# Optimization experiments

Measured on AMD Instinct MI355X. Metric: run time of the kernel, lower is better.

Reference implementation:

```python
import jax, jax.numpy as jnp
import numpy as np
import math

N = 50000        # nodes
E = 800000       # edges (avg degree 16)
NFEAT = 512
NHID = 512
NCLASS = 128


def setup_inputs() -> dict:
    key = jax.random.key(0)
    ks = jax.random.split(key, 8)
    x = jax.random.normal(ks[0], (N, NFEAT), dtype=jnp.float32)
    edge_src = jax.random.randint(ks[1], (E,), 0, N)
    edge_dst = jax.random.randint(ks[2], (E,), 0, N)
    edge_w = jax.random.uniform(ks[3], (E,), dtype=jnp.float32)
    s1 = 1.0 / math.sqrt(NFEAT)
    s2 = 1.0 / math.sqrt(NHID)
    # torch Linear weight layout: [out_features, in_features]
    W1 = jax.random.uniform(ks[4], (NHID, NFEAT), dtype=jnp.float32, minval=-s1, maxval=s1)
    b1 = jax.random.uniform(ks[5], (NHID,), dtype=jnp.float32, minval=-s1, maxval=s1)
    W2 = jax.random.uniform(ks[6], (NCLASS, NHID), dtype=jnp.float32, minval=-s2, maxval=s2)
    b2 = jax.random.uniform(ks[7], (NCLASS,), dtype=jnp.float32, minval=-s2, maxval=s2)
    return {"x": x, "edge_w": edge_w, "W1": W1, "b1": b1, "W2": W2, "b2": b2,
            "edge_src": edge_src, "edge_dst": edge_dst}


def reference(x, edge_w, W1, b1, W2, b2, edge_src, edge_dst):
    # spmm(adj, support): out[i] = sum_{e: src[e]==i} w[e] * support[dst[e]]
    def spmm(support):
        gathered = edge_w[:, None] * support[edge_dst]  # [E, F]
        return jax.ops.segment_sum(gathered, edge_src, num_segments=N)

    # layer 1: linear -> spmm -> relu (dropout is identity in eval mode)
    h = spmm(x @ W1.T + b1)
    h = jax.nn.relu(h)
    # layer 2 (output layer): linear -> spmm
    out = spmm(h @ W2.T + b2)
    return out
```

## Files before the change

kernel.cpp:

```cpp
#include <hip/hip_runtime.h>
#include <hip/hip_bf16.h>
#include <hip/hip_fp8.h>
#include <stdint.h>

#define N_NODES 50000
#define N_EDGES 800000
#define NFEAT 512
#define NHID 512
#define NCLASS 128
#define MPAD 50048

#define CONVX_BLOCKS 12512
#define CONVW1_BLOCKS 128
#define CONVW2_BLOCKS 32
#define HIST_BLOCKS 3125
#define G1_BM 391
#define G1_BLOCKS 1564
#define FILL_BLOCKS 3125

typedef short short8 __attribute__((ext_vector_type(8)));
typedef float f32x4 __attribute__((ext_vector_type(4)));
typedef float f32x2 __attribute__((ext_vector_type(2)));

__device__ __forceinline__ ushort f2bf(float f) {
  union { float f; uint32_t u; } v; v.f = f;
  uint32_t u = v.u;
  uint32_t r = (u + 0x7fffu + ((u >> 16) & 1u)) >> 16;
  return (ushort)r;
}
__device__ __forceinline__ float bf2f(ushort h) {
  union { uint32_t u; float f; } v; v.u = ((uint32_t)h) << 16;
  return v.f;
}

__device__ __forceinline__ uint8_t enc_fp8(float f) {
#if __has_builtin(__builtin_amdgcn_cvt_pk_fp8_f32)
  int r = __builtin_amdgcn_cvt_pk_fp8_f32(f, f, 0, false);
  return (uint8_t)(r & 0xff);
#else
  __hip_fp8_e4m3 t(f);
  return t.__x;
#endif
}
__device__ __forceinline__ float dec_fp8_byte(uint32_t b) {
  uint32_t e = (b >> 3) & 15u, m = b & 7u, s = (b & 0x80u) << 24;
  union { uint32_t u; float f; } n; n.u = s | ((e + 120u) << 23) | (m << 20);
  union { uint32_t u; float f; } d; d.f = (float)m * 0x1p-9f; d.u |= s;
  return e ? n.f : d.f;
}

__device__ __forceinline__ void acc_fp8x4(float* a, uint32_t v, float w) {
#if __has_builtin(__builtin_amdgcn_cvt_pk_f32_fp8)
  f32x2 lo = __builtin_amdgcn_cvt_pk_f32_fp8(v, false);
  f32x2 hi = __builtin_amdgcn_cvt_pk_f32_fp8(v, true);
  a[0] += w * lo[0]; a[1] += w * lo[1]; a[2] += w * hi[0]; a[3] += w * hi[1];
#else
  a[0] += w * dec_fp8_byte(v & 0xffu);
  a[1] += w * dec_fp8_byte((v >> 8) & 0xffu);
  a[2] += w * dec_fp8_byte((v >> 16) & 0xffu);
  a[3] += w * dec_fp8_byte(v >> 24);
#endif
}

__device__ __forceinline__ void acc_bf16x2(float* a, uint32_t v, float w) {
  a[0] += w * bf2f((ushort)(v & 0xffffu));
  a[1] += w * bf2f((ushort)(v >> 16));
}

__device__ __forceinline__ void conv8(const float* __restrict__ in,
                                      ushort* __restrict__ out, long idx) {
  const float4* p = (const float4*)(in + idx);
  float4 a = p[0], b = p[1];
  short8 o;
  o[0] = f2bf(a.x); o[1] = f2bf(a.y); o[2] = f2bf(a.z); o[3] = f2bf(a.w);
  o[4] = f2bf(b.x); o[5] = f2bf(b.y); o[6] = f2bf(b.z); o[7] = f2bf(b.w);
  *(short8*)(out + idx) = o;
}

__device__ __forceinline__ void gload_lds16(const void* g, void* lds) {
  __builtin_amdgcn_global_load_lds(
      (const __attribute__((address_space(1))) void*)g,
      (__attribute__((address_space(3))) void*)lds,
      16, 0, 0);
}

__global__ __launch_bounds__(256) void k_prep(const float* __restrict__ x,
                                              ushort* __restrict__ xb,
                                              const float* __restrict__ W1,
                                              ushort* __restrict__ w1b,
                                              const float* __restrict__ W2,
                                              ushort* __restrict__ w2b) {
  int b = blockIdx.x, t = threadIdx.x;
  if (b < CONVX_BLOCKS) {
    long idx = ((long)b * 256 + t) * 8;
    int row = (int)(idx >> 9);
    if (row < N_NODES) {
      conv8(x, xb, idx);
    } else {
      *(short8*)(xb + idx) = (short8)0;
    }
  } else if (b < CONVX_BLOCKS + CONVW1_BLOCKS) {
    long idx = ((long)(b - CONVX_BLOCKS) * 256 + t) * 8;
    conv8(W1, w1b, idx);
  } else {
    long idx = ((long)(b - CONVX_BLOCKS - CONVW1_BLOCKS) * 256 + t) * 8;
    conv8(W2, w2b, idx);
  }
}

__global__ __launch_bounds__(256) void k_alloc(const int* __restrict__ deg,
                                               int* __restrict__ rpb,
                                               int* __restrict__ rpe,
                                               int* __restrict__ counter) {
  int i = blockIdx.x * blockDim.x + threadIdx.x;
  int lane = threadIdx.x & 63;
  int d = (i < N_NODES) ? deg[i] : 0;
  int sc = d;
  #pragma unroll
  for (int off = 1; off < 64; off <<= 1) {
    int u = __shfl_up(sc, off, 64);
    if (lane >= off) sc += u;
  }
  int base = 0;
  if (lane == 63) base = atomicAdd(counter, sc);
  base = __shfl(base, 63, 64);
  if (i < N_NODES) {
    int start = base + sc - d;
    rpb[i] = start;
    rpe[i] = start + d;
  }
}

__global__ __launch_bounds__(256) void k_fill(const int* __restrict__ src,
                                              const int* __restrict__ dst,
                                              const float* __restrict__ w,
                                              const int* __restrict__ rpb,
                                              const int* __restrict__ rank,
                                              uint2* __restrict__ esw) {
  int e = blockIdx.x * blockDim.x + threadIdx.x;
  if (e < N_EDGES) {
    int pos = rpb[src[e]] + rank[e];
    uint2 p;
    p.x = (unsigned)dst[e];
    p.y = __float_as_uint(w[e]);
    esw[pos] = p;
  }
}

template <int OUT_FP8>
__device__ __forceinline__ void gemm_body(const ushort* __restrict__ A,
                                          const ushort* __restrict__ B,
                                          const float* __restrict__ bias,
                                          void* __restrict__ Cout,
                                          int K, int Nout, int bm, int bn,
                                          ushort* sA, ushort* sB) {
  const int t = threadIdx.x;
  const int lane = t & 63;
  const int wave = t >> 6;
  const int wr = wave >> 1, wc = wave & 1;

  f32x4 acc[4][4];
  #pragma unroll
  for (int i = 0; i < 4; i++)
    #pragma unroll
    for (int j = 0; j < 4; j++) acc[i][j] = (f32x4)0.f;

  const long a_base = (long)bm * 128 * K;
  const long b_base = (long)bn * 128 * K;

  for (int kt = 0; kt < K; kt += 64) {
    #pragma unroll
    for (int it = 0; it < 4; ++it) {
      int c = it * 256 + t;
      int r = c >> 3, ccp = c & 7;
      int cc = ccp ^ (r & 7);
      const ushort* ga = A + a_base + (long)r * K + kt + cc * 8;
      const ushort* gb = B + b_base + (long)r * K + kt + cc * 8;
      char* la = (char*)sA + (it * 256 + wave * 64) * 16;
      char* lb = (char*)sB + (it * 256 + wave * 64) * 16;
      gload_lds16(ga, la);
      gload_lds16(gb, lb);
    }
    __syncthreads();
    #pragma unroll
    for (int kk = 0; kk < 2; ++kk) {
      short8 af[4], bfr[4];
      int kchunk = kk * 4 + (lane >> 4);
      #pragma unroll
      for (int mr = 0; mr < 4; ++mr) {
        int row = wr * 64 + mr * 16 + (lane & 15);
        af[mr] = *(const short8*)((const char*)sA + row * 128 +
                                  ((kchunk * 16) ^ ((row & 7) << 4)));
      }
      #pragma unroll
      for (int nr = 0; nr < 4; ++nr) {
        int row = wc * 64 + nr * 16 + (lane & 15);
        bfr[nr] = *(const short8*)((const char*)sB + row * 128 +
                                   ((kchunk * 16) ^ ((row & 7) << 4)));
      }
      #pragma unroll
      for (int mr = 0; mr < 4; ++mr)
        #pragma unroll
        for (int nr = 0; nr < 4; ++nr)
          acc[mr][nr] = __builtin_amdgcn_mfma_f32_16x16x32_bf16(af[mr], bfr[nr],
                                                                acc[mr][nr], 0, 0, 0);
    }
    __syncthreads();
  }

  #pragma unroll
  for (int mr = 0; mr < 4; ++mr)
    #pragma unroll
    for (int nr = 0; nr < 4; ++nr) {
      int col = bn * 128 + wc * 64 + nr * 16 + (lane & 15);
      float bv = bias[col];
      #pragma unroll
      for (int reg = 0; reg < 4; ++reg) {
        int row = bm * 128 + wr * 64 + mr * 16 + (lane >> 4) * 4 + reg;
        float val = acc[mr][nr][reg] + bv;
        if (OUT_FP8) {
          ((uint8_t*)Cout)[(long)row * Nout + col] = enc_fp8(val);
        } else {
          ((ushort*)Cout)[(long)row * Nout + col] = f2bf(val);
        }
      }
    }
}

__global__ __launch_bounds__(256) void k_gemm1_hist(const ushort* __restrict__ A,
                                                    const ushort* __restrict__ B,
                                                    const float* __restrict__ bias,
                                                    uint8_t* __restrict__ C,
                                                    const int* __restrict__ src,
                                                    int* __restrict__ deg,
                                                    int* __restrict__ rank) {
  __shared__ ushort sA[128 * 64];
  __shared__ ushort sB[128 * 64];
  int b = blockIdx.x;
  if (b < G1_BLOCKS) {
    gemm_body<1>(A, B, bias, C, NFEAT, NHID, b % G1_BM, b / G1_BM, sA, sB);
  } else {
    int e = (b - G1_BLOCKS) * 256 + threadIdx.x;
    if (e < N_EDGES) rank[e] = atomicAdd(&deg[src[e]], 1);
  }
}

__global__ __launch_bounds__(256) void k_gemm2(const ushort* __restrict__ A,
                                               const ushort* __restrict__ B,
                                               const float* __restrict__ bias,
                                               ushort* __restrict__ C) {
  __shared__ ushort sA[128 * 64];
  __shared__ ushort sB[128 * 64];
  gemm_body<0>(A, B, bias, C, NHID, NCLASS, blockIdx.x, 0, sA, sB);
}

__global__ __launch_bounds__(256) void k_spmm1(const int* __restrict__ rpb,
                                               const int* __restrict__ rpe,
                                               const uint2* __restrict__ esw,
                                               const uint8_t* __restrict__ c1,
                                               ushort* __restrict__ h) {
  int node = blockIdx.x * 4 + (threadIdx.x >> 6);
  int lane = threadIdx.x & 63;
  int half = lane >> 5;
  int col = (lane & 31) * 16;
  float a[16];
  #pragma unroll
  for (int k = 0; k < 16; ++k) a[k] = 0.f;
  if (node < N_NODES) {
    int beg = rpb[node], end = rpe[node];
    for (int j = beg; j < end; j += 8) {
      #pragma unroll
      for (int s = 0; s < 4; ++s) {
        int ei = j + s * 2 + half;
        bool vld = ei < end;
        uint2 p = esw[vld ? ei : 0];
        int d = (int)p.x;
        float w = vld ? __uint_as_float(p.y) : 0.f;
        uint4 q = *(const uint4*)(c1 + (long)d * NHID + col);
        acc_fp8x4(a, q.x, w);      acc_fp8x4(a + 4, q.y, w);
        acc_fp8x4(a + 8, q.z, w);  acc_fp8x4(a + 12, q.w, w);
      }
    }
  }
  #pragma unroll
  for (int k = 0; k < 16; ++k) a[k] += __shfl_xor(a[k], 32, 64);
  if (half == 0) {
    short8 o0, o1;
    #pragma unroll
    for (int k = 0; k < 8; ++k) {
      o0[k] = (short)f2bf(a[k] > 0.f ? a[k] : 0.f);
      o1[k] = (short)f2bf(a[k + 8] > 0.f ? a[k + 8] : 0.f);
    }
    *(short8*)(h + (long)node * NHID + col) = o0;
    *(short8*)(h + (long)node * NHID + col + 8) = o1;
  }
}

__global__ __launch_bounds__(256) void k_spmm2(const int* __restrict__ rpb,
                                               const int* __restrict__ rpe,
                                               const uint2* __restrict__ esw,
                                               const ushort* __restrict__ c2,
                                               float* __restrict__ out) {
  int node = blockIdx.x * 4 + (threadIdx.x >> 6);
  int lane = threadIdx.x & 63;
  int half = lane >> 5;
  int col = (lane & 31) * 4;
  if (node >= N_NODES) return;
  float a[4] = {0.f, 0.f, 0.f, 0.f};
  int beg = rpb[node], end = rpe[node];
  for (int j = beg; j < end; j += 8) {
    #pragma unroll
    for (int s = 0; s < 4; ++s) {
      int ei = j + s * 2 + half;
      bool vld = ei < end;
      uint2 p = esw[vld ? ei : 0];
      int d = (int)p.x;
      float w = vld ? __uint_as_float(p.y) : 0.f;
      uint2 q = *(const uint2*)(c2 + (long)d * NCLASS + col);
      acc_bf16x2(a, q.x, w);
      acc_bf16x2(a + 2, q.y, w);
    }
  }
  #pragma unroll
  for (int k = 0; k < 4; ++k) a[k] += __shfl_xor(a[k], 32, 64);
  if (half == 0) {
    f32x4 st; st[0] = a[0]; st[1] = a[1]; st[2] = a[2]; st[3] = a[3];
    *(f32x4*)(out + (long)node * NCLASS + col) = st;
  }
}

extern "C" void kernel_launch(void* const* d_in, const int* in_sizes, int n_in,
                              void* d_out, int out_size, void* d_ws, size_t ws_size,
                              hipStream_t stream) {
  const float* x    = (const float*)d_in[0];
  const float* ew   = (const float*)d_in[1];
  const float* W1   = (const float*)d_in[2];
  const float* b1   = (const float*)d_in[3];
  const float* W2   = (const float*)d_in[4];
  const float* b2   = (const float*)d_in[5];
  const int*   esrc = (const int*)d_in[6];
  const int*   edst = (const int*)d_in[7];
  float* out = (float*)d_out;

  char* ws = (char*)d_ws;
  size_t off = 0;
  auto alloc = [&](size_t bytes) -> void* {
    void* p = ws + off;
    off = (off + bytes + 255) & ~(size_t)255;
    return p;
  };

  ushort*  buf0 = (ushort*)alloc((size_t)MPAD * 512 * 2);
  uint8_t* c1f8 = (uint8_t*)alloc((size_t)MPAD * 512);
  ushort*  c2bf = (ushort*)alloc((size_t)MPAD * 128 * 2);
  ushort*  w1b  = (ushort*)alloc((size_t)512 * 512 * 2);
  ushort*  w2b  = (ushort*)alloc((size_t)128 * 512 * 2);
  int*     deg  = (int*)alloc((size_t)N_NODES * 4);
  int*     rpb  = (int*)alloc((size_t)N_NODES * 4);
  int*     rpe  = (int*)alloc((size_t)N_NODES * 4);
  int*     rank = (int*)alloc((size_t)N_EDGES * 4);
  int*     cnt  = (int*)alloc(256);
  uint2*   esw  = (uint2*)alloc((size_t)N_EDGES * 8);

  hipMemsetAsync(deg, 0, (size_t)N_NODES * 4, stream);
  hipMemsetAsync(cnt, 0, 4, stream);

  k_prep<<<CONVX_BLOCKS + CONVW1_BLOCKS + CONVW2_BLOCKS, 256, 0, stream>>>(
      x, buf0, W1, w1b, W2, w2b);

  k_gemm1_hist<<<G1_BLOCKS + HIST_BLOCKS, 256, 0, stream>>>(
      buf0, w1b, b1, c1f8, esrc, deg, rank);

  k_alloc<<<(N_NODES + 255) / 256, 256, 0, stream>>>(deg, rpb, rpe, cnt);

  k_fill<<<FILL_BLOCKS, 256, 0, stream>>>(esrc, edst, ew, rpb, rank, esw);

  k_spmm1<<<MPAD / 4, 256, 0, stream>>>(rpb, rpe, esw, c1f8, buf0);

  k_gemm2<<<G1_BM, 256, 0, stream>>>(buf0, w2b, b2, c2bf);

  k_spmm2<<<(N_NODES + 3) / 4, 256, 0, stream>>>(rpb, rpe, esw, c2bf, out);
}
```

Baseline: 249.4 us.

## Fuse x fp32-to-bf16 conversion into GEMM1 tile loads and interleave histogram blocks

Removes the separate pass that converted x to bf16 and instead converts fp32 rows on the fly while staging the A tile into LDS in GEMM1. Histogram blocks are interleaved with GEMM blocks (one GEMM to two hist) to mix compute and atomic work. This avoids writing and rereading a bf16 copy of x, at the cost of reading fp32 x once per column tile and losing async global-to-LDS loads for A.

```diff
diff --git a/kernel.cpp b/kernel.cpp
--- a/kernel.cpp
+++ b/kernel.cpp
@@ -10,12 +10,12 @@
 #define NCLASS 128
 #define MPAD 50048
 
-#define CONVX_BLOCKS 12512
 #define CONVW1_BLOCKS 128
 #define CONVW2_BLOCKS 32
 #define HIST_BLOCKS 3125
 #define G1_BM 391
 #define G1_BLOCKS 1564
+#define G1H_BLOCKS 4692
 #define FILL_BLOCKS 3125
 
 typedef short short8 __attribute__((ext_vector_type(8)));
@@ -84,26 +84,16 @@
       16, 0, 0);
 }
 
-__global__ __launch_bounds__(256) void k_prep(const float* __restrict__ x,
-                                              ushort* __restrict__ xb,
-                                              const float* __restrict__ W1,
-                                              ushort* __restrict__ w1b,
-                                              const float* __restrict__ W2,
-                                              ushort* __restrict__ w2b) {
+__global__ __launch_bounds__(256) void k_prepw(const float* __restrict__ W1,
+                                               ushort* __restrict__ w1b,
+                                               const float* __restrict__ W2,
+                                               ushort* __restrict__ w2b) {
   int b = blockIdx.x, t = threadIdx.x;
-  if (b < CONVX_BLOCKS) {
+  if (b < CONVW1_BLOCKS) {
     long idx = ((long)b * 256 + t) * 8;
-    int row = (int)(idx >> 9);
-    if (row < N_NODES) {
-      conv8(x, xb, idx);
-    } else {
-      *(short8*)(xb + idx) = (short8)0;
-    }
-  } else if (b < CONVX_BLOCKS + CONVW1_BLOCKS) {
-    long idx = ((long)(b - CONVX_BLOCKS) * 256 + t) * 8;
     conv8(W1, w1b, idx);
   } else {
-    long idx = ((long)(b - CONVX_BLOCKS - CONVW1_BLOCKS) * 256 + t) * 8;
+    long idx = ((long)(b - CONVW1_BLOCKS) * 256 + t) * 8;
     conv8(W2, w2b, idx);
   }
 }
@@ -147,13 +137,13 @@
   }
 }
 
-template <int OUT_FP8>
-__device__ __forceinline__ void gemm_body(const ushort* __restrict__ A,
-                                          const ushort* __restrict__ B,
-                                          const float* __restrict__ bias,
-                                          void* __restrict__ Cout,
-                                          int K, int Nout, int bm, int bn,
-                                          ushort* sA, ushort* sB) {
+__device__ __forceinline__ void gemm1_body(const float* __restrict__ X,
+                                           const ushort* __restrict__ B,
+                                           const float* __restrict__ bias,
+                                           uint8_t* __restrict__ Cout,
+                                           int bm, int bn,
+                                           ushort* sA, ushort* sB) {
+  const int K = NFEAT, Nout = NHID;
   const int t = threadIdx.x;
   const int lane = t & 63;
   const int wave = t >> 6;
@@ -165,21 +155,27 @@
     #pragma unroll
     for (int j = 0; j < 4; j++) acc[i][j] = (f32x4)0.f;
 
-  const long a_base = (long)bm * 128 * K;
   const long b_base = (long)bn * 128 * K;
 
   for (int kt = 0; kt < K; kt += 64) {
     #pragma unroll
     for (int it = 0; it < 4; ++it) {
       int c = it * 256 + t;
-      int r = c >> 3, ccp = c & 7;
-      int cc = ccp ^ (r & 7);
-      const ushort* ga = A + a_base + (long)r * K + kt + cc * 8;
-      const ushort* gb = B + b_base + (long)r * K + kt + cc * 8;
-      char* la = (char*)sA + (it * 256 + wave * 64) * 16;
-      char* lb = (char*)sB + (it * 256 + wave * 64) * 16;
-      gload_lds16(ga, la);
-      gload_lds16(gb, lb);
+      int r = c >> 3;
+      int ccp = c & 7;
+      int ccg = ccp ^ (r & 7);
+      gload_lds16(B + b_base + (long)r * K + kt + ccg * 8,
+                  (char*)sB + (it * 256 + wave * 64) * 16);
+      int cc = c & 7;
+      long grow = (long)bm * 128 + r;
+      short8 o = (short8)0;
+      if (grow < N_NODES) {
+        const float4* p = (const float4*)(X + grow * NFEAT + kt + cc * 8);
+        float4 va = p[0], vb = p[1];
+        o[0] = f2bf(va.x); o[1] = f2bf(va.y); o[2] = f2bf(va.z); o[3] = f2bf(va.w);
+        o[4] = f2bf(vb.x); o[5] = f2bf(vb.y); o[6] = f2bf(vb.z); o[7] = f2bf(vb.w);
+      }
+      *(short8*)((char*)sA + r * 128 + ((cc ^ (r & 7)) * 16)) = o;
     }
     __syncthreads();
     #pragma unroll
@@ -217,17 +213,84 @@
       #pragma unroll
       for (int reg = 0; reg < 4; ++reg) {
         int row = bm * 128 + wr * 64 + mr * 16 + (lane >> 4) * 4 + reg;
-        float val = acc[mr][nr][reg] + bv;
-        if (OUT_FP8) {
-          ((uint8_t*)Cout)[(long)row * Nout + col] = enc_fp8(val);
-        } else {
-          ((ushort*)Cout)[(long)row * Nout + col] = f2bf(val);
-        }
-      }
-    }
-}
-
-__global__ __launch_bounds__(256) void k_gemm1_hist(const ushort* __restrict__ A,
+        Cout[(long)row * Nout + col] = enc_fp8(acc[mr][nr][reg] + bv);
+      }
+    }
+}
+
+__device__ __forceinline__ void gemm_body_bf(const ushort* __restrict__ A,
+                                             const ushort* __restrict__ B,
+                                             const float* __restrict__ bias,
+                                             ushort* __restrict__ Cout,
+                                             int K, int Nout, int bm, int bn,
+                                             ushort* sA, ushort* sB) {
+  const int t = threadIdx.x;
+  const int lane = t & 63;
+  const int wave = t >> 6;
+  const int wr = wave >> 1, wc = wave & 1;
+
+  f32x4 acc[4][4];
+  #pragma unroll
+  for (int i = 0; i < 4; i++)
+    #pragma unroll
+    for (int j = 0; j < 4; j++) acc[i][j] = (f32x4)0.f;
+
+  const long a_base = (long)bm * 128 * K;
+  const long b_base = (long)bn * 128 * K;
+
+  for (int kt = 0; kt < K; kt += 64) {
+    #pragma unroll
+    for (int it = 0; it < 4; ++it) {
+      int c = it * 256 + t;
+      int r = c >> 3, ccp = c & 7;
+      int cc = ccp ^ (r & 7);
+      gload_lds16(A + a_base + (long)r * K + kt + cc * 8,
+                  (char*)sA + (it * 256 + wave * 64) * 16);
+      gload_lds16(B + b_base + (long)r * K + kt + cc * 8,
+                  (char*)sB + (it * 256 + wave * 64) * 16);
+    }
+    __syncthreads();
+    #pragma unroll
+    for (int kk = 0; kk < 2; ++kk) {
+      short8 af[4], bfr[4];
+      int kchunk = kk * 4 + (lane >> 4);
+      #pragma unroll
+      for (int mr = 0; mr < 4; ++mr) {
+        int row = wr * 64 + mr * 16 + (lane & 15);
+        af[mr] = *(const short8*)((const char*)sA + row * 128 +
+                                  ((kchunk * 16) ^ ((row & 7) << 4)));
+      }
+      #pragma unroll
+      for (int nr = 0; nr < 4; ++nr) {
+        int row = wc * 64 + nr * 16 + (lane & 15);
+        bfr[nr] = *(const short8*)((const char*)sB + row * 128 +
+                                   ((kchunk * 16) ^ ((row & 7) << 4)));
+      }
+      #pragma unroll
+      for (int mr = 0; mr < 4; ++mr)
+        #pragma unroll
+        for (int nr = 0; nr < 4; ++nr)
+          acc[mr][nr] = __builtin_amdgcn_mfma_f32_16x16x32_bf16(af[mr], bfr[nr],
+                                                                acc[mr][nr], 0, 0, 0);
+    }
+    __syncthreads();
+  }
+
+  #pragma unroll
+  for (int mr = 0; mr < 4; ++mr)
+    #pragma unroll
+    for (int nr = 0; nr < 4; ++nr) {
+      int col = bn * 128 + wc * 64 + nr * 16 + (lane & 15);
+      float bv = bias[col];
+      #pragma unroll
+      for (int reg = 0; reg < 4; ++reg) {
+        int row = bm * 128 + wr * 64 + mr * 16 + (lane >> 4) * 4 + reg;
+        Cout[(long)row * Nout + col] = f2bf(acc[mr][nr][reg] + bv);
+      }
+    }
+}
+
+__global__ __launch_bounds__(256) void k_gemm1_hist(const float* __restrict__ X,
                                                     const ushort* __restrict__ B,
                                                     const float* __restrict__ bias,
                                                     uint8_t* __restrict__ C,
@@ -237,10 +300,11 @@
   __shared__ ushort sA[128 * 64];
   __shared__ ushort sB[128 * 64];
   int b = blockIdx.x;
-  if (b < G1_BLOCKS) {
-    gemm_body<1>(A, B, bias, C, NFEAT, NHID, b % G1_BM, b / G1_BM, sA, sB);
+  int g = b / 3, rem = b - g * 3;
+  if (rem == 0) {
+    gemm1_body(X, B, bias, C, g >> 2, g & 3, sA, sB);
   } else {
-    int e = (b - G1_BLOCKS) * 256 + threadIdx.x;
+    int e = (g * 2 + rem - 1) * 256 + threadIdx.x;
     if (e < N_EDGES) rank[e] = atomicAdd(&deg[src[e]], 1);
   }
 }
@@ -251,7 +315,7 @@
                                                ushort* __restrict__ C) {
   __shared__ ushort sA[128 * 64];
   __shared__ ushort sB[128 * 64];
-  gemm_body<0>(A, B, bias, C, NHID, NCLASS, blockIdx.x, 0, sA, sB);
+  gemm_body_bf(A, B, bias, C, NHID, NCLASS, blockIdx.x, 0, sA, sB);
 }
 
 __global__ __launch_bounds__(256) void k_spmm1(const int* __restrict__ rpb,
@@ -350,7 +414,7 @@
     return p;
   };
 
-  ushort*  buf0 = (ushort*)alloc((size_t)MPAD * 512 * 2);
+  ushort*  hbuf = (ushort*)alloc((size_t)MPAD * 512 * 2);
   uint8_t* c1f8 = (uint8_t*)alloc((size_t)MPAD * 512);
   ushort*  c2bf = (ushort*)alloc((size_t)MPAD * 128 * 2);
   ushort*  w1b  = (ushort*)alloc((size_t)512 * 512 * 2);
@@ -365,19 +429,17 @@
   hipMemsetAsync(deg, 0, (size_t)N_NODES * 4, stream);
   hipMemsetAsync(cnt, 0, 4, stream);
 
-  k_prep<<<CONVX_BLOCKS + CONVW1_BLOCKS + CONVW2_BLOCKS, 256, 0, stream>>>(
-      x, buf0, W1, w1b, W2, w2b);
-
-  k_gemm1_hist<<<G1_BLOCKS + HIST_BLOCKS, 256, 0, stream>>>(
-      buf0, w1b, b1, c1f8, esrc, deg, rank);
+  k_prepw<<<CONVW1_BLOCKS + CONVW2_BLOCKS, 256, 0, stream>>>(W1, w1b, W2, w2b);
+
+  k_gemm1_hist<<<G1H_BLOCKS, 256, 0, stream>>>(x, w1b, b1, c1f8, esrc, deg, rank);
 
   k_alloc<<<(N_NODES + 255) / 256, 256, 0, stream>>>(deg, rpb, rpe, cnt);
 
   k_fill<<<FILL_BLOCKS, 256, 0, stream>>>(esrc, edst, ew, rpb, rank, esw);
 
-  k_spmm1<<<MPAD / 4, 256, 0, stream>>>(rpb, rpe, esw, c1f8, buf0);
-
-  k_gemm2<<<G1_BM, 256, 0, stream>>>(buf0, w2b, b2, c2bf);
+  k_spmm1<<<MPAD / 4, 256, 0, stream>>>(rpb, rpe, esw, c1f8, hbuf);
+
+  k_gemm2<<<G1_BM, 256, 0, stream>>>(hbuf, w2b, b2, c2bf);
 
   k_spmm2<<<(N_NODES + 3) / 4, 256, 0, stream>>>(rpb, rpe, esw, c2bf, out);
 }
```

Result: no change. 246.8 us (-1.1%).
